# Performance work log

Hardware: AMD Instinct MI355X
Metric: run time of the kernel (lower is better)

The kernel has to match this reference:

```python
import jax, jax.numpy as jnp
import numpy as np

IN_CH = 1024   # backbone channels
N_T = 81       # n_targets (COCO classes + bg)
K = 7          # PSROI grid size
H = 100        # feature map height
WID = 100      # feature map width
R = 1024       # number of regions
S = 2          # bilinear sampling points per bin edge (PSROIAlign-style average)


def setup_inputs() -> dict:
    key = jax.random.key(0)
    k1, k2, k3 = jax.random.split(key, 3)
    x = jax.random.normal(k1, (IN_CH, H, WID), dtype=jnp.float32)
    # regions: fractional (i, j, h, w) = (center_y, center_x, height, width) in [0,1]
    regions = jax.random.uniform(k2, (R, 4), dtype=jnp.float32)
    conv_w = jax.random.normal(k3, (N_T * K * K, IN_CH), dtype=jnp.float32) * 0.02
    conv_b = jnp.zeros((N_T * K * K,), dtype=jnp.float32)
    return {"x": x, "regions": regions, "conv_w": conv_w, "conv_b": conv_b}


def _bilinear_pool(map_thw, ys, xs):
    """Average of bilinear samples of one bin's score map.

    map_thw: (T, H, W) score map for this (u, v) bin's channel group.
    ys: (R, S) sample row coords.  xs: (R, S) sample col coords.
    Returns (R, T): per-region average-pooled bin value.
    """
    Hm, Wm = map_thw.shape[1], map_thw.shape[2]
    ys = jnp.clip(ys, 0.0, Hm - 1)
    xs = jnp.clip(xs, 0.0, Wm - 1)
    y0 = jnp.floor(ys)
    x0 = jnp.floor(xs)
    y0i = y0.astype(jnp.int32)
    x0i = x0.astype(jnp.int32)
    y1i = jnp.minimum(y0i + 1, Hm - 1)
    x1i = jnp.minimum(x0i + 1, Wm - 1)
    wy1 = ys - y0
    wy0 = 1.0 - wy1
    wx1 = xs - x0
    wx0 = 1.0 - wx1

    def g(yi, xi):  # gather (T, R, S, S)
        return map_thw[:, yi[:, :, None], xi[:, None, :]]

    v = (g(y0i, x0i) * (wy0[:, :, None] * wx0[:, None, :])
         + g(y0i, x1i) * (wy0[:, :, None] * wx1[:, None, :])
         + g(y1i, x0i) * (wy1[:, :, None] * wx0[:, None, :])
         + g(y1i, x1i) * (wy1[:, :, None] * wx1[:, None, :]))
    return v.mean((2, 3)).T  # (R, T)


def reference(x, regions, conv_w, conv_b):
    # 1x1 conv score map: (n_targets*k^2, H, W)
    sm = jnp.einsum('oc,chw->ohw', conv_w, x) + conv_b[:, None, None]
    sm = sm.reshape(N_T, K, K, H, WID)  # (T, ky, kx, H, W) position-sensitive groups

    # region geometry (fractional center/size -> absolute feature-map coords)
    top = (regions[:, 0] - regions[:, 2] * 0.5) * H     # (R,)
    left = (regions[:, 1] - regions[:, 3] * 0.5) * WID  # (R,)
    bh = regions[:, 2] * H / K                          # bin height
    bw = regions[:, 3] * WID / K                        # bin width

    off = (jnp.arange(S, dtype=jnp.float32) + 0.5) / S  # (S,) sample offsets in bin
    bins = jnp.arange(K, dtype=jnp.float32)             # (K,)
    ys = top[:, None, None] + (bins[None, :, None] + off[None, None, :]) * bh[:, None, None]   # (R,K,S)
    xs = left[:, None, None] + (bins[None, :, None] + off[None, None, :]) * bw[:, None, None]  # (R,K,S)

    # vmap over the k x k position-sensitive bins; bin (u,v) reads channel group (:,u,v)
    inner = jax.vmap(_bilinear_pool, in_axes=(1, None, 1))  # over kx: sm axis, xs axis
    outer = jax.vmap(inner, in_axes=(1, 1, None))           # over ky: sm axis, ys axis
    pooled = outer(sm, ys, xs)  # (K, K, R, T)

    # pooled.mean(-1).mean(-1) over the k x k grid
    scores = pooled.mean((0, 1))  # (R, T)
    return scores
```

## Files before the change

### kernel.cpp

```cpp
#include <hip/hip_runtime.h>
#include <cstddef>

#define IN_CH 1024
#define NT    81
#define KGRID 7
#define NBINS 49
#define HH    100
#define WW    100
#define NPIX  (HH*WW)
#define NREG  1024
#define COLB  82
#define NCOL  (NBINS*COLB)
#define NPADW 4096
#define NG    8

typedef unsigned short ushortT;
typedef short bf16x8 __attribute__((ext_vector_type(8)));
typedef float f32x4  __attribute__((ext_vector_type(4)));

static __device__ __forceinline__ unsigned short f2bf(float f) {
    unsigned int u = __builtin_bit_cast(unsigned int, f);
    return (unsigned short)((u + 0x7fffu + ((u >> 16) & 1u)) >> 16);
}
static __device__ __forceinline__ float bf_lo(unsigned int v) {
    return __builtin_bit_cast(float, v << 16);
}
static __device__ __forceinline__ float bf_hi(unsigned int v) {
    return __builtin_bit_cast(float, v & 0xffff0000u);
}

static __device__ __forceinline__ void gld_lds16(const ushortT* g, ushortT* l) {
    __builtin_amdgcn_global_load_lds(
        (__attribute__((address_space(1))) void*)(unsigned long long)(uintptr_t)g,
        (__attribute__((address_space(3))) void*)(unsigned int)(unsigned long long)(uintptr_t)l,
        16, 0, 0);
}

__global__ __launch_bounds__(256) void prep_x(const float* __restrict__ x,
                                              ushortT* __restrict__ xbT) {
    __shared__ float tile[128][33];
    const int tid = threadIdx.x;
    const int p0 = blockIdx.x * 32;
    const int c0 = blockIdx.y * 128;
    const int pl = tid & 31;
    const int cg = tid >> 5;
    const int p = p0 + pl;
#pragma unroll
    for (int it = 0; it < 16; ++it) {
        const int c = it * 8 + cg;
        tile[c][pl] = (p < NPIX) ? x[(size_t)(c0 + c) * NPIX + p] : 0.0f;
    }
    __syncthreads();
#pragma unroll
    for (int pass = 0; pass < 2; ++pass) {
        const int pix = pass * 16 + (tid >> 4);
        const int cb  = (tid & 15) * 8;
        if (p0 + pix < NPIX) {
            uint4 pk;
            pk.x = (unsigned int)f2bf(tile[cb + 0][pix]) | ((unsigned int)f2bf(tile[cb + 1][pix]) << 16);
            pk.y = (unsigned int)f2bf(tile[cb + 2][pix]) | ((unsigned int)f2bf(tile[cb + 3][pix]) << 16);
            pk.z = (unsigned int)f2bf(tile[cb + 4][pix]) | ((unsigned int)f2bf(tile[cb + 5][pix]) << 16);
            pk.w = (unsigned int)f2bf(tile[cb + 6][pix]) | ((unsigned int)f2bf(tile[cb + 7][pix]) << 16);
            *(uint4*)(xbT + (size_t)(p0 + pix) * IN_CH + c0 + cb) = pk;
        }
    }
}

__global__ __launch_bounds__(256) void prep_w(const float* __restrict__ conv_w,
                                              ushortT* __restrict__ Wr) {
    const int row = blockIdx.x;
    const int bin = row / COLB;
    const int t   = row - bin * COLB;
    const int c   = threadIdx.x * 4;
    uint2 pk; pk.x = 0; pk.y = 0;
    if (bin < NBINS && t < NT) {
        const float4 v = *(const float4*)(conv_w + ((size_t)(t * NBINS + bin)) * IN_CH + c);
        pk.x = (unsigned int)f2bf(v.x) | ((unsigned int)f2bf(v.y) << 16);
        pk.y = (unsigned int)f2bf(v.z) | ((unsigned int)f2bf(v.w) << 16);
    }
    *(uint2*)(Wr + (size_t)row * IN_CH + c) = pk;
}

__global__ __launch_bounds__(256) void gemm_sm(const ushortT* __restrict__ xbT,
                                               const ushortT* __restrict__ Wr,
                                               ushortT* __restrict__ sm) {
    __shared__ ushortT a_lds[128 * 32];
    __shared__ ushortT b_lds[128 * 32];
    const int tid  = threadIdx.x;
    const int lane = tid & 63;
    const int w    = tid >> 6;
    const int wm   = w & 1;
    const int wn   = w >> 1;
    const int n0   = blockIdx.x * 128;
    const int p0   = blockIdx.y * 128;

    const int srow0 = w * 32 + (lane >> 2);
    const int scol  = (lane & 3) * 8;
    int ap0 = p0 + srow0;      if (ap0 > NPIX - 1) ap0 = NPIX - 1;
    int ap1 = p0 + srow0 + 16; if (ap1 > NPIX - 1) ap1 = NPIX - 1;
    const ushortT* ag0 = xbT + (size_t)ap0 * IN_CH + scol;
    const ushortT* ag1 = xbT + (size_t)ap1 * IN_CH + scol;
    const ushortT* bg0 = Wr + (size_t)(n0 + srow0) * IN_CH + scol;
    const ushortT* bg1 = Wr + (size_t)(n0 + srow0 + 16) * IN_CH + scol;
    ushortT* al0 = a_lds + (w * 32) * 32;
    ushortT* al1 = a_lds + (w * 32 + 16) * 32;
    ushortT* bl0 = b_lds + (w * 32) * 32;
    ushortT* bl1 = b_lds + (w * 32 + 16) * 32;

    const int m_lane = lane & 15;
    const int k0     = (lane >> 4) * 8;

    f32x4 acc[4][4];
#pragma unroll
    for (int mt = 0; mt < 4; ++mt)
#pragma unroll
        for (int nt = 0; nt < 4; ++nt) acc[mt][nt] = (f32x4){0.f, 0.f, 0.f, 0.f};

    for (int kc = 0; kc < IN_CH / 32; ++kc) {
        __syncthreads();
        gld_lds16(ag0, al0);
        gld_lds16(ag1, al1);
        gld_lds16(bg0, bl0);
        gld_lds16(bg1, bl1);
        ag0 += 32; ag1 += 32; bg0 += 32; bg1 += 32;
        __syncthreads();

        bf16x8 af[4], bf[4];
#pragma unroll
        for (int mt = 0; mt < 4; ++mt)
            af[mt] = *(const bf16x8*)(a_lds + (wm * 64 + mt * 16 + m_lane) * 32 + k0);
#pragma unroll
        for (int nt = 0; nt < 4; ++nt)
            bf[nt] = *(const bf16x8*)(b_lds + (wn * 64 + nt * 16 + m_lane) * 32 + k0);
#pragma unroll
        for (int mt = 0; mt < 4; ++mt)
#pragma unroll
            for (int nt = 0; nt < 4; ++nt)
                acc[mt][nt] = __builtin_amdgcn_mfma_f32_16x16x32_bf16(af[mt], bf[nt], acc[mt][nt], 0, 0, 0);
    }

    const int prow_base = p0 + wm * 64 + (lane >> 4) * 4;
    const int ncol_base = n0 + wn * 64 + m_lane;
#pragma unroll
    for (int nt = 0; nt < 4; ++nt) {
        const int n = ncol_base + nt * 16;
        if (n < NCOL) {
            const int bin = n / COLB;
            const int t   = n - bin * COLB;
            ushortT* colp = sm + (size_t)bin * NPIX * COLB + t;
#pragma unroll
            for (int mt = 0; mt < 4; ++mt) {
#pragma unroll
                for (int rg = 0; rg < 4; ++rg) {
                    const int p = prow_base + mt * 16 + rg;
                    if (p < NPIX) colp[(size_t)p * COLB] = f2bf(acc[nt][mt * 0 + 0][0] * 0.0f + acc[mt][nt][rg]);
                }
            }
        }
    }
}

__global__ __launch_bounds__(256) void pool_kernel(const ushortT* __restrict__ sm,
                                                   const float* __restrict__ regions,
                                                   const float* __restrict__ conv_b,
                                                   float* __restrict__ out) {
    __shared__ int   rowo[28]; __shared__ float roww[28];
    __shared__ int   coli[28]; __shared__ float colw[28];
    __shared__ int   pofs_l[98];
    __shared__ float pw_l[98];
    __shared__ float part[4][COLB];
    const int tid = threadIdx.x;
    const int b = blockIdx.x;
    const int g = b >> 10;
    const int r = b & (NREG - 1);

    if (tid < 28) {
        const float4 reg = *(const float4*)(regions + (size_t)r * 4);
        const float top = (reg.x - reg.z * 0.5f) * (float)HH;
        const float bh  = reg.z * ((float)HH / (float)KGRID);
        const int u = tid >> 2, i = tid & 3;
        const int s = i >> 1, hi = i & 1;
        float y = top + ((float)u + ((float)s + 0.5f) * 0.5f) * bh;
        y = fminf(fmaxf(y, 0.0f), (float)(HH - 1));
        const float y0f = floorf(y);
        const int y0 = (int)y0f;
        const float wy1 = y - y0f;
        rowo[tid] = (hi ? min(y0 + 1, HH - 1) : y0) * WW;
        roww[tid] = hi ? wy1 : (1.0f - wy1);
    } else if (tid >= 32 && tid < 60) {
        const float4 reg = *(const float4*)(regions + (size_t)r * 4);
        const float left = (reg.y - reg.w * 0.5f) * (float)WW;
        const float bw   = reg.w * ((float)WW / (float)KGRID);
        const int idx = tid - 32;
        const int v = idx >> 2, j = idx & 3;
        const int s = j >> 1, hi = j & 1;
        float xx = left + ((float)v + ((float)s + 0.5f) * 0.5f) * bw;
        xx = fminf(fmaxf(xx, 0.0f), (float)(WW - 1));
        const float x0f = floorf(xx);
        const int x0 = (int)x0f;
        const float wx1 = xx - x0f;
        coli[idx] = hi ? min(x0 + 1, WW - 1) : x0;
        colw[idx] = hi ? wx1 : (1.0f - wx1);
    }
    __syncthreads();
    if (tid < 98) {
        const int tt = g * 98 + tid;
        const int bin = tt >> 4, tap = tt & 15;
        const int u = bin / KGRID, v = bin - u * KGRID;
        const int i = tap >> 2, j = tap & 3;
        const int pix = rowo[u * 4 + i] + coli[v * 4 + j];
        pofs_l[tid] = (bin * NPIX + pix) * COLB;
        pw_l[tid]   = roww[u * 4 + i] * colw[v * 4 + j] * (1.0f / 196.0f);
    }
    __syncthreads();

    const int lane = tid & 63, w = tid >> 6;
    if (lane < COLB / 2) {
        float a0 = 0.f, a1 = 0.f;
        const int l2 = lane * 2;
#pragma unroll
        for (int it = 0; it < 25; ++it) {
            const int lt = it * 4 + w;
            if (lt < 98) {
                const unsigned int v = *(const unsigned int*)(sm + pofs_l[lt] + l2);
                const float wt = pw_l[lt];
                a0 += wt * bf_lo(v);
                a1 += wt * bf_hi(v);
            }
        }
        part[w][l2] = a0; part[w][l2 + 1] = a1;
    }
    __syncthreads();
    if (tid < NT) {
        float v = part[0][tid] + part[1][tid] + part[2][tid] + part[3][tid];
        if (g == 0) {
            float bsum = 0.f;
            for (int bin = 0; bin < NBINS; ++bin) bsum += conv_b[tid * NBINS + bin];
            v += bsum * (1.0f / (float)NBINS);
        }
        atomicAdd(out + (size_t)r * NT + tid, v);
    }
}

__global__ __launch_bounds__(256) void xpose_kernel(const float* __restrict__ x,
                                                    float* __restrict__ xt) {
    __shared__ float tile[32][33];
    const int p0 = blockIdx.x * 32;
    const int c0 = blockIdx.y * 32;
    const int tx = threadIdx.x;
    const int ty = threadIdx.y;
#pragma unroll
    for (int k = 0; k < 32; k += 8) {
        const int p = p0 + tx;
        if (p < NPIX) tile[ty + k][tx] = x[(size_t)(c0 + ty + k) * NPIX + p];
    }
    __syncthreads();
#pragma unroll
    for (int k = 0; k < 32; k += 8) {
        const int p = p0 + ty + k;
        if (p < NPIX) xt[(size_t)p * IN_CH + (c0 + tx)] = tile[tx][ty + k];
    }
}

template <bool XPOSED>
__global__ __launch_bounds__(256) void psroi_kernel(
    const float* __restrict__ xsrc, const float* __restrict__ regions,
    const float* __restrict__ conv_w, const float* __restrict__ conv_b,
    float* __restrict__ out) {
    __shared__ float w_lds[32 * 96];
    __shared__ float g_lds[32 * 64];
    __shared__ int   rowoff[64][4];
    __shared__ float rowwf[64][4];
    __shared__ int   colidx[64][4];
    __shared__ float colwf[64][4];
    const int tid = threadIdx.x;
    const int bin = blockIdx.x >> 4;
    const int rg  = blockIdx.x & 15;
    const int u = bin / KGRID, v = bin % KGRID;
    const int r0 = rg * 64;
    if (tid < 64) {
        const float4 reg = *(const float4*)(regions + (size_t)(r0 + tid) * 4);
        const float top  = (reg.x - reg.z * 0.5f) * (float)HH;
        const float left = (reg.y - reg.w * 0.5f) * (float)WW;
        const float bh = reg.z * ((float)HH / (float)KGRID);
        const float bw = reg.w * ((float)WW / (float)KGRID);
        const float scale = 1.0f / 196.0f;
#pragma unroll
        for (int s = 0; s < 2; s++) {
            const float off = (s + 0.5f) * 0.5f;
            float yy = top + ((float)u + off) * bh;
            yy = fminf(fmaxf(yy, 0.0f), (float)(HH - 1));
            const float y0f = floorf(yy);
            const int y0 = (int)y0f;
            const float wy1 = yy - y0f;
            rowoff[tid][2 * s] = y0 * WW;
            rowoff[tid][2 * s + 1] = min(y0 + 1, HH - 1) * WW;
            rowwf[tid][2 * s] = (1.0f - wy1) * scale;
            rowwf[tid][2 * s + 1] = wy1 * scale;
            float xx = left + ((float)v + off) * bw;
            xx = fminf(fmaxf(xx, 0.0f), (float)(WW - 1));
            const float x0f = floorf(xx);
            const int x0 = (int)x0f;
            const float wx1 = xx - x0f;
            colidx[tid][2 * s] = x0;
            colidx[tid][2 * s + 1] = min(x0 + 1, WW - 1);
            colwf[tid][2 * s] = 1.0f - wx1;
            colwf[tid][2 * s + 1] = wx1;
        }
    }
    const int ri = tid & 15, tq = tid >> 4, rb = tid >> 2, cq = tid & 3;
    float acc[4][6];
#pragma unroll
    for (int m = 0; m < 4; m++)
#pragma unroll
        for (int k = 0; k < 6; k++) acc[m][k] = 0.0f;
    for (int chunk = 0; chunk < IN_CH / 32; chunk++) {
        const int c0 = chunk * 32;
        __syncthreads();
#pragma unroll
        for (int it = 0; it < 12; it++) {
            const int idx = it * 256 + tid;
            const int t = idx >> 5, c = idx & 31;
            float val = 0.0f;
            if (t < NT) val = conv_w[(size_t)(t * NBINS + bin) * IN_CH + c0 + c];
            w_lds[c * 96 + t] = val;
        }
        const int cbase = c0 + cq * 8;
        float g8[8];
#pragma unroll
        for (int cc = 0; cc < 8; cc++) g8[cc] = 0.0f;
#pragma unroll
        for (int i = 0; i < 4; i++) {
            const int ro = rowoff[rb][i];
            const float wy = rowwf[rb][i];
#pragma unroll
            for (int j = 0; j < 4; j++) {
                const int pix = ro + colidx[rb][j];
                const float wv = wy * colwf[rb][j];
                if (XPOSED) {
                    const float4* p = (const float4*)(xsrc + (size_t)pix * IN_CH + cbase);
                    const float4 a = p[0]; const float4 b = p[1];
                    g8[0] += wv * a.x; g8[1] += wv * a.y; g8[2] += wv * a.z; g8[3] += wv * a.w;
                    g8[4] += wv * b.x; g8[5] += wv * b.y; g8[6] += wv * b.z; g8[7] += wv * b.w;
                } else {
#pragma unroll
                    for (int cc = 0; cc < 8; cc++)
                        g8[cc] += wv * xsrc[(size_t)(cbase + cc) * NPIX + pix];
                }
            }
        }
#pragma unroll
        for (int cc = 0; cc < 8; cc++) g_lds[(cq * 8 + cc) * 64 + rb] = g8[cc];
        __syncthreads();
#pragma unroll 4
        for (int c = 0; c < 32; c++) {
            float wv[6];
#pragma unroll
            for (int k = 0; k < 6; k++) wv[k] = w_lds[c * 96 + tq * 6 + k];
            const float4 gq = *(const float4*)&g_lds[c * 64 + ri * 4];
            const float gm[4] = {gq.x, gq.y, gq.z, gq.w};
#pragma unroll
            for (int m = 0; m < 4; m++)
#pragma unroll
                for (int k = 0; k < 6; k++) acc[m][k] += gm[m] * wv[k];
        }
    }
    const float invK2 = 1.0f / 49.0f;
#pragma unroll
    for (int k = 0; k < 6; k++) {
        const int t = tq * 6 + k;
        if (t < NT) {
            const float bterm = conv_b[t * NBINS + bin] * invK2;
#pragma unroll
            for (int m = 0; m < 4; m++) {
                const int rr = r0 + ri * 4 + m;
                atomicAdd(&out[(size_t)rr * NT + t], acc[m][k] + bterm);
            }
        }
    }
}

extern "C" void kernel_launch(void* const* d_in, const int* in_sizes, int n_in,
                              void* d_out, int out_size, void* d_ws, size_t ws_size,
                              hipStream_t stream) {
    const float* x       = (const float*)d_in[0];
    const float* regions = (const float*)d_in[1];
    const float* conv_w  = (const float*)d_in[2];
    const float* conv_b  = (const float*)d_in[3];
    float* out = (float*)d_out;

    const size_t sz_xbT = (size_t)NPIX * IN_CH * 2;
    const size_t sz_Wr  = (size_t)NPADW * IN_CH * 2;
    const size_t sz_sm  = (size_t)NBINS * NPIX * COLB * 2;
    const size_t need   = sz_xbT + sz_Wr + sz_sm;

    if (ws_size >= need) {
        ushortT* xbT = (ushortT*)d_ws;
        ushortT* Wr  = (ushortT*)((char*)d_ws + sz_xbT);
        ushortT* sm  = (ushortT*)((char*)d_ws + sz_xbT + sz_Wr);
        hipMemsetAsync(out, 0, (size_t)out_size * sizeof(float), stream);
        prep_x<<<dim3((NPIX + 31) / 32, IN_CH / 128), 256, 0, stream>>>(x, xbT);
        prep_w<<<dim3(NPADW), 256, 0, stream>>>(conv_w, Wr);
        gemm_sm<<<dim3(NPADW / 128, (NPIX + 127) / 128), 256, 0, stream>>>(xbT, Wr, sm);
        pool_kernel<<<dim3(NG * NREG), 256, 0, stream>>>(sm, regions, conv_b, out);
    } else {
        hipMemsetAsync(out, 0, (size_t)out_size * sizeof(float), stream);
        const size_t xt_bytes = (size_t)NPIX * IN_CH * sizeof(float);
        const dim3 mainGrid(NBINS * 16);
        if (ws_size >= xt_bytes) {
            float* xt = (float*)d_ws;
            xpose_kernel<<<dim3((NPIX + 31) / 32, IN_CH / 32), dim3(32, 8), 0, stream>>>(x, xt);
            psroi_kernel<true><<<mainGrid, 256, 0, stream>>>(xt, regions, conv_w, conv_b, out);
        } else {
            psroi_kernel<false><<<mainGrid, 256, 0, stream>>>(x, regions, conv_w, conv_b, out);
        }
    }
}
```

Measured before the change: 251.5 us.

## Switch score map to pixel-major layout, fuse prep kernels, one pool block per region

Merges the x-transpose and weight-conversion kernels into a single launch and changes the score-map layout from bin-major to pixel-major rows (pixel × all bin columns). The GEMM epilogue now writes contiguous columns along a pixel row. The pooling kernel handles one region per block over all 784 taps with 6 thread groups, so the atomics and the memset are no longer needed. This cuts launch count and atomic traffic and makes the epilogue stores more contiguous, at the cost of fewer and longer pool blocks with scattered per-tap reads.

```diff
diff --git a/kernel.cpp b/kernel.cpp
--- a/kernel.cpp
+++ b/kernel.cpp
@@ -12,7 +12,10 @@
 #define COLB  82
 #define NCOL  (NBINS*COLB)
 #define NPADW 4096
-#define NG    8
+#define SROW  NCOL
+#define PXB   ((NPIX + 31) / 32)
+#define PXG   (PXB * (IN_CH / 128))
+#define PREPG (PXG + NPADW)
 
 typedef unsigned short ushortT;
 typedef short bf16x8 __attribute__((ext_vector_type(8)));
@@ -36,49 +39,51 @@
         16, 0, 0);
 }
 
-__global__ __launch_bounds__(256) void prep_x(const float* __restrict__ x,
-                                              ushortT* __restrict__ xbT) {
+__global__ __launch_bounds__(256) void prep_fused(const float* __restrict__ x,
+                                                  ushortT* __restrict__ xbT,
+                                                  const float* __restrict__ conv_w,
+                                                  ushortT* __restrict__ Wr) {
     __shared__ float tile[128][33];
     const int tid = threadIdx.x;
-    const int p0 = blockIdx.x * 32;
-    const int c0 = blockIdx.y * 128;
-    const int pl = tid & 31;
-    const int cg = tid >> 5;
-    const int p = p0 + pl;
-#pragma unroll
-    for (int it = 0; it < 16; ++it) {
-        const int c = it * 8 + cg;
-        tile[c][pl] = (p < NPIX) ? x[(size_t)(c0 + c) * NPIX + p] : 0.0f;
-    }
-    __syncthreads();
-#pragma unroll
-    for (int pass = 0; pass < 2; ++pass) {
-        const int pix = pass * 16 + (tid >> 4);
-        const int cb  = (tid & 15) * 8;
-        if (p0 + pix < NPIX) {
-            uint4 pk;
-            pk.x = (unsigned int)f2bf(tile[cb + 0][pix]) | ((unsigned int)f2bf(tile[cb + 1][pix]) << 16);
-            pk.y = (unsigned int)f2bf(tile[cb + 2][pix]) | ((unsigned int)f2bf(tile[cb + 3][pix]) << 16);
-            pk.z = (unsigned int)f2bf(tile[cb + 4][pix]) | ((unsigned int)f2bf(tile[cb + 5][pix]) << 16);
-            pk.w = (unsigned int)f2bf(tile[cb + 6][pix]) | ((unsigned int)f2bf(tile[cb + 7][pix]) << 16);
-            *(uint4*)(xbT + (size_t)(p0 + pix) * IN_CH + c0 + cb) = pk;
-        }
-    }
-}
-
-__global__ __launch_bounds__(256) void prep_w(const float* __restrict__ conv_w,
-                                              ushortT* __restrict__ Wr) {
-    const int row = blockIdx.x;
-    const int bin = row / COLB;
-    const int t   = row - bin * COLB;
-    const int c   = threadIdx.x * 4;
-    uint2 pk; pk.x = 0; pk.y = 0;
-    if (bin < NBINS && t < NT) {
-        const float4 v = *(const float4*)(conv_w + ((size_t)(t * NBINS + bin)) * IN_CH + c);
-        pk.x = (unsigned int)f2bf(v.x) | ((unsigned int)f2bf(v.y) << 16);
-        pk.y = (unsigned int)f2bf(v.z) | ((unsigned int)f2bf(v.w) << 16);
-    }
-    *(uint2*)(Wr + (size_t)row * IN_CH + c) = pk;
+    const int bid = blockIdx.x;
+    if (bid < PXG) {
+        const int p0 = (bid % PXB) * 32;
+        const int c0 = (bid / PXB) * 128;
+        const int pl = tid & 31;
+        const int cg = tid >> 5;
+        const int p = p0 + pl;
+#pragma unroll
+        for (int it = 0; it < 16; ++it) {
+            const int c = it * 8 + cg;
+            tile[c][pl] = (p < NPIX) ? x[(size_t)(c0 + c) * NPIX + p] : 0.0f;
+        }
+        __syncthreads();
+#pragma unroll
+        for (int pass = 0; pass < 2; ++pass) {
+            const int pix = pass * 16 + (tid >> 4);
+            const int cb  = (tid & 15) * 8;
+            if (p0 + pix < NPIX) {
+                uint4 pk;
+                pk.x = (unsigned int)f2bf(tile[cb + 0][pix]) | ((unsigned int)f2bf(tile[cb + 1][pix]) << 16);
+                pk.y = (unsigned int)f2bf(tile[cb + 2][pix]) | ((unsigned int)f2bf(tile[cb + 3][pix]) << 16);
+                pk.z = (unsigned int)f2bf(tile[cb + 4][pix]) | ((unsigned int)f2bf(tile[cb + 5][pix]) << 16);
+                pk.w = (unsigned int)f2bf(tile[cb + 6][pix]) | ((unsigned int)f2bf(tile[cb + 7][pix]) << 16);
+                *(uint4*)(xbT + (size_t)(p0 + pix) * IN_CH + c0 + cb) = pk;
+            }
+        }
+    } else {
+        const int row = bid - PXG;
+        const int bin = row / COLB;
+        const int t   = row - bin * COLB;
+        const int c   = tid * 4;
+        uint2 pk; pk.x = 0; pk.y = 0;
+        if (bin < NBINS && t < NT) {
+            const float4 v = *(const float4*)(conv_w + ((size_t)(t * NBINS + bin)) * IN_CH + c);
+            pk.x = (unsigned int)f2bf(v.x) | ((unsigned int)f2bf(v.y) << 16);
+            pk.y = (unsigned int)f2bf(v.z) | ((unsigned int)f2bf(v.w) << 16);
+        }
+        *(uint2*)(Wr + (size_t)row * IN_CH + c) = pk;
+    }
 }
 
 __global__ __launch_bounds__(256) void gemm_sm(const ushortT* __restrict__ xbT,
@@ -142,18 +147,16 @@
     const int prow_base = p0 + wm * 64 + (lane >> 4) * 4;
     const int ncol_base = n0 + wn * 64 + m_lane;
 #pragma unroll
-    for (int nt = 0; nt < 4; ++nt) {
-        const int n = ncol_base + nt * 16;
-        if (n < NCOL) {
-            const int bin = n / COLB;
-            const int t   = n - bin * COLB;
-            ushortT* colp = sm + (size_t)bin * NPIX * COLB + t;
-#pragma unroll
-            for (int mt = 0; mt < 4; ++mt) {
-#pragma unroll
-                for (int rg = 0; rg < 4; ++rg) {
-                    const int p = prow_base + mt * 16 + rg;
-                    if (p < NPIX) colp[(size_t)p * COLB] = f2bf(acc[nt][mt * 0 + 0][0] * 0.0f + acc[mt][nt][rg]);
+    for (int mt = 0; mt < 4; ++mt) {
+#pragma unroll
+        for (int rg = 0; rg < 4; ++rg) {
+            const int p = prow_base + mt * 16 + rg;
+            if (p < NPIX) {
+                ushortT* rowp = sm + (size_t)p * SROW;
+#pragma unroll
+                for (int nt = 0; nt < 4; ++nt) {
+                    const int n = ncol_base + nt * 16;
+                    if (n < NCOL) rowp[n] = f2bf(acc[mt][nt][rg]);
                 }
             }
         }
@@ -166,13 +169,11 @@
                                                    float* __restrict__ out) {
     __shared__ int   rowo[28]; __shared__ float roww[28];
     __shared__ int   coli[28]; __shared__ float colw[28];
-    __shared__ int   pofs_l[98];
-    __shared__ float pw_l[98];
-    __shared__ float part[4][COLB];
+    __shared__ int   pofs[784];
+    __shared__ float pw[784];
+    __shared__ float part[6][COLB];
     const int tid = threadIdx.x;
-    const int b = blockIdx.x;
-    const int g = b >> 10;
-    const int r = b & (NREG - 1);
+    const int r = blockIdx.x;
 
     if (tid < 28) {
         const float4 reg = *(const float4*)(regions + (size_t)r * 4);
@@ -203,42 +204,36 @@
         colw[idx] = hi ? wx1 : (1.0f - wx1);
     }
     __syncthreads();
-    if (tid < 98) {
-        const int tt = g * 98 + tid;
+    for (int tt = tid; tt < 784; tt += 256) {
         const int bin = tt >> 4, tap = tt & 15;
         const int u = bin / KGRID, v = bin - u * KGRID;
         const int i = tap >> 2, j = tap & 3;
         const int pix = rowo[u * 4 + i] + coli[v * 4 + j];
-        pofs_l[tid] = (bin * NPIX + pix) * COLB;
-        pw_l[tid]   = roww[u * 4 + i] * colw[v * 4 + j] * (1.0f / 196.0f);
+        pofs[tt] = pix * SROW + bin * COLB;
+        pw[tt]   = roww[u * 4 + i] * colw[v * 4 + j] * (1.0f / 196.0f);
     }
     __syncthreads();
 
-    const int lane = tid & 63, w = tid >> 6;
-    if (lane < COLB / 2) {
+    const int tg    = tid / 41;
+    const int cslot = tid - tg * 41;
+    if (tg < 6) {
         float a0 = 0.f, a1 = 0.f;
-        const int l2 = lane * 2;
-#pragma unroll
-        for (int it = 0; it < 25; ++it) {
-            const int lt = it * 4 + w;
-            if (lt < 98) {
-                const unsigned int v = *(const unsigned int*)(sm + pofs_l[lt] + l2);
-                const float wt = pw_l[lt];
-                a0 += wt * bf_lo(v);
-                a1 += wt * bf_hi(v);
-            }
-        }
-        part[w][l2] = a0; part[w][l2 + 1] = a1;
+        const int l2 = cslot * 2;
+        for (int lt = tg; lt < 784; lt += 6) {
+            const unsigned int v = *(const unsigned int*)(sm + pofs[lt] + l2);
+            const float wt = pw[lt];
+            a0 += wt * bf_lo(v);
+            a1 += wt * bf_hi(v);
+        }
+        part[tg][l2] = a0; part[tg][l2 + 1] = a1;
     }
     __syncthreads();
     if (tid < NT) {
-        float v = part[0][tid] + part[1][tid] + part[2][tid] + part[3][tid];
-        if (g == 0) {
-            float bsum = 0.f;
-            for (int bin = 0; bin < NBINS; ++bin) bsum += conv_b[tid * NBINS + bin];
-            v += bsum * (1.0f / (float)NBINS);
-        }
-        atomicAdd(out + (size_t)r * NT + tid, v);
+        float v = part[0][tid] + part[1][tid] + part[2][tid]
+                + part[3][tid] + part[4][tid] + part[5][tid];
+        float bsum = 0.f;
+        for (int bin = 0; bin < NBINS; ++bin) bsum += conv_b[tid * NBINS + bin];
+        out[(size_t)r * NT + tid] = v + bsum * (1.0f / (float)NBINS);
     }
 }
 
@@ -391,18 +386,16 @@
 
     const size_t sz_xbT = (size_t)NPIX * IN_CH * 2;
     const size_t sz_Wr  = (size_t)NPADW * IN_CH * 2;
-    const size_t sz_sm  = (size_t)NBINS * NPIX * COLB * 2;
+    const size_t sz_sm  = (size_t)NPIX * SROW * 2;
     const size_t need   = sz_xbT + sz_Wr + sz_sm;
 
     if (ws_size >= need) {
         ushortT* xbT = (ushortT*)d_ws;
         ushortT* Wr  = (ushortT*)((char*)d_ws + sz_xbT);
         ushortT* sm  = (ushortT*)((char*)d_ws + sz_xbT + sz_Wr);
-        hipMemsetAsync(out, 0, (size_t)out_size * sizeof(float), stream);
-        prep_x<<<dim3((NPIX + 31) / 32, IN_CH / 128), 256, 0, stream>>>(x, xbT);
-        prep_w<<<dim3(NPADW), 256, 0, stream>>>(conv_w, Wr);
+        prep_fused<<<dim3(PREPG), 256, 0, stream>>>(x, xbT, conv_w, Wr);
         gemm_sm<<<dim3(NPADW / 128, (NPIX + 127) / 128), 256, 0, stream>>>(xbT, Wr, sm);
-        pool_kernel<<<dim3(NG * NREG), 256, 0, stream>>>(sm, regions, conv_b, out);
+        pool_kernel<<<dim3(NREG), 256, 0, stream>>>(sm, regions, conv_b, out);
     } else {
         hipMemsetAsync(out, 0, (size_t)out_size * sizeof(float), stream);
         const size_t xt_bytes = (size_t)NPIX * IN_CH * sizeof(float);
```

Result: slower. 261.9 us (+4.1%).
